# Kernel tuning notes

Hardware: AMD Instinct MI355X
Metric: run time of the kernel (lower is better)

The kernel has to match this reference:

```python
import jax, jax.numpy as jnp
import numpy as np
import math

HIDDEN_DIM = 1024
N_HEAD = 16
HEAD_DIM = HIDDEN_DIM // N_HEAD
BS, SEQ = 2, 4096


def setup_inputs() -> dict:
    key = jax.random.key(0)
    ks = jax.random.split(key, 6)
    s = 1.0 / math.sqrt(HIDDEN_DIM)
    return {
        "x": jax.random.normal(ks[0], (BS, SEQ, HIDDEN_DIM), dtype=jnp.float32),
        "attention_mask": jnp.zeros((1, 1, SEQ, SEQ), dtype=jnp.float32),
        "wq_w": jax.random.normal(ks[1], (HIDDEN_DIM, HIDDEN_DIM), dtype=jnp.float32) * s,
        "wq_b": jnp.zeros((HIDDEN_DIM,), dtype=jnp.float32),
        "wk_w": jax.random.normal(ks[2], (HIDDEN_DIM, HIDDEN_DIM), dtype=jnp.float32) * s,
        "wk_b": jnp.zeros((HIDDEN_DIM,), dtype=jnp.float32),
        "wv_w": jax.random.normal(ks[3], (HIDDEN_DIM, HIDDEN_DIM), dtype=jnp.float32) * s,
        "wv_b": jnp.zeros((HIDDEN_DIM,), dtype=jnp.float32),
        "wo_w": jax.random.normal(ks[4], (HIDDEN_DIM, HIDDEN_DIM), dtype=jnp.float32) * s,
        "wo_b": jnp.zeros((HIDDEN_DIM,), dtype=jnp.float32),
    }


def reference(x, attention_mask, wq_w, wq_b, wk_w, wk_b, wv_w, wv_b, wo_w, wo_b):
    bs, seq_len, _ = x.shape
    # nn.Linear: y = x @ W.T + b
    Q = x @ wq_w.T + wq_b
    K = x @ wk_w.T + wk_b
    V = x @ wv_w.T + wv_b
    # [bs, n_head, seq, head_dim]
    Q = Q.reshape(bs, seq_len, N_HEAD, HEAD_DIM).transpose(0, 2, 1, 3)
    K = K.reshape(bs, seq_len, N_HEAD, HEAD_DIM).transpose(0, 2, 1, 3)
    V = V.reshape(bs, seq_len, N_HEAD, HEAD_DIM).transpose(0, 2, 1, 3)
    scale = 1.0 / math.sqrt(HEAD_DIM)
    att = jnp.einsum('bhqd,bhkd->bhqk', Q, K) * scale
    att = att + attention_mask
    att = jax.nn.softmax(att, axis=-1)
    # dropout is identity in eval mode (p=0.1 during training)
    out = jnp.einsum('bhqk,bhkd->bhqd', att, V)
    out = out.transpose(0, 2, 1, 3).reshape(bs, seq_len, HIDDEN_DIM)
    return out @ wo_w.T + wo_b
```

## Files before the change

### kernel.cpp

```cpp
#include <hip/hip_runtime.h>

typedef unsigned short u16;
typedef __bf16 bf16x4 __attribute__((ext_vector_type(4)));
typedef __bf16 bf16x8 __attribute__((ext_vector_type(8)));
typedef float f32x4 __attribute__((ext_vector_type(4)));

#define SEQ_LEN 4096
#define HID 1024
#define NHEAD 16
#define HDIM 64
#define MROWS 8192
#define LOG2E 1.44269504088896f

__device__ __forceinline__ u16 f2bf(float f) {
  union { float f; unsigned u; } v; v.f = f;
  unsigned r = v.u + 0x7fffu + ((v.u >> 16) & 1u);
  return (u16)(r >> 16);
}

__device__ __forceinline__ float fexp2(float x) {
  float r;
  asm("v_exp_f32 %0, %1" : "=v"(r) : "v"(x));
  return r;
}

__device__ __forceinline__ bf16x8 pack8(f32x4 a, f32x4 b) {
  union { unsigned u[4]; bf16x8 v; } r;
  asm("v_cvt_pk_bf16_f32 %0, %1, %2" : "=v"(r.u[0]) : "v"(a[0]), "v"(a[1]));
  asm("v_cvt_pk_bf16_f32 %0, %1, %2" : "=v"(r.u[1]) : "v"(a[2]), "v"(a[3]));
  asm("v_cvt_pk_bf16_f32 %0, %1, %2" : "=v"(r.u[2]) : "v"(b[0]), "v"(b[1]));
  asm("v_cvt_pk_bf16_f32 %0, %1, %2" : "=v"(r.u[3]) : "v"(b[2]), "v"(b[3]));
  return r.v;
}

__device__ __forceinline__ void gload16(const void* g, void* lds) {
  __builtin_amdgcn_global_load_lds((const __attribute__((address_space(1))) void*)g,
                                   (__attribute__((address_space(3))) void*)lds, 16, 0, 0);
}


__global__ void prep_kernel(const float* __restrict__ x,
                            const float* __restrict__ w0, const float* __restrict__ w1,
                            const float* __restrict__ w2, const float* __restrict__ w3,
                            const float* __restrict__ mask,
                            u16* __restrict__ xb, u16* __restrict__ wb, int* __restrict__ flag) {
  const int NX = MROWS * HID / 4;
  const int NW = HID * HID / 4;
  const int NM = SEQ_LEN * SEQ_LEN / 4;
  const int TOT = NX + 4 * NW + NM;
  int stride = gridDim.x * blockDim.x;
  bool nz = false;
  for (int i = blockIdx.x * blockDim.x + threadIdx.x; i < TOT; i += stride) {
    if (i < NX) {
      float4 v = ((const float4*)x)[i];
      ((ushort4*)xb)[i] = make_ushort4(f2bf(v.x), f2bf(v.y), f2bf(v.z), f2bf(v.w));
    } else if (i < NX + 4 * NW) {
      int j = i - NX;
      int mat = j >> 18;
      int off = j & (NW - 1);
      const float* src = (mat == 0) ? w0 : (mat == 1) ? w1 : (mat == 2) ? w2 : w3;
      float4 v = ((const float4*)src)[off];
      ((ushort4*)(wb + (size_t)mat * HID * HID))[off] =
          make_ushort4(f2bf(v.x), f2bf(v.y), f2bf(v.z), f2bf(v.w));
    } else {
      int j = i - NX - 4 * NW;
      float4 v = ((const float4*)mask)[j];
      nz |= (v.x != 0.f) | (v.y != 0.f) | (v.z != 0.f) | (v.w != 0.f);
    }
  }
  if (__any(nz) && (threadIdx.x & 63) == 0) atomicOr(flag, 1);
}


__device__ __forceinline__ void gemm_core(const u16* __restrict__ A, const u16* __restrict__ W,
                                          int m0, int n0, char* As, char* Bs, f32x4 acc[4][4]) {
  const int t = threadIdx.x, w = t >> 6, l = t & 63;
  const int lr = l & 15, lg = l >> 4;
  const int wr = (w >> 1) * 64, wc = (w & 1) * 64;
#pragma unroll
  for (int i = 0; i < 4; i++)
#pragma unroll
    for (int j = 0; j < 4; j++) acc[i][j] = (f32x4){0.f, 0.f, 0.f, 0.f};

  for (int k0 = 0; k0 < HID; k0 += 64) {
    __syncthreads();
#pragma unroll
    for (int j = 0; j < 4; j++) {
      int o = w * 4096 + j * 1024 + l * 16;
      int row = o >> 7, kb = (o >> 4) & 7, skb = kb ^ (row & 7);
      gload16(A + (size_t)(m0 + row) * HID + k0 + skb * 8, As + (w * 4096 + j * 1024));
      gload16(W + (size_t)(n0 + row) * HID + k0 + skb * 8, Bs + (w * 4096 + j * 1024));
    }
    __syncthreads();
#pragma unroll
    for (int ks = 0; ks < 2; ks++) {
      bf16x8 af[4], bf[4];
      int kb = ks * 4 + lg;
#pragma unroll
      for (int mt = 0; mt < 4; mt++) {
        int row = wr + mt * 16 + lr;
        af[mt] = *(const bf16x8*)(As + row * 128 + ((kb ^ (row & 7)) << 4));
      }
#pragma unroll
      for (int nt = 0; nt < 4; nt++) {
        int row = wc + nt * 16 + lr;
        bf[nt] = *(const bf16x8*)(Bs + row * 128 + ((kb ^ (row & 7)) << 4));
      }
#pragma unroll
      for (int mt = 0; mt < 4; mt++)
#pragma unroll
        for (int nt = 0; nt < 4; nt++)
          acc[mt][nt] = __builtin_amdgcn_mfma_f32_16x16x32_bf16(af[mt], bf[nt], acc[mt][nt], 0, 0, 0);
    }
  }
}

__global__ __launch_bounds__(256) void gemm_qkv_kernel(
    const u16* __restrict__ xb, const u16* __restrict__ wqb, const u16* __restrict__ wkb,
    const u16* __restrict__ wvb, const float* __restrict__ bq, const float* __restrict__ bk,
    const float* __restrict__ bv, u16* __restrict__ Qb, u16* __restrict__ Kb, u16* __restrict__ VT) {
  __shared__ __align__(128) char lds[32768];
  int flat = blockIdx.y * 64 + blockIdx.x;
  int xcd = flat & 7, j = flat >> 3;
  int bx = xcd * 8 + (j & 7);
  int by = j >> 3;
  int m0 = bx * 128;
  int ng = by * 128;
  int mat = ng >> 10, n0 = ng & 1023;
  const u16* W = (mat == 0) ? wqb : (mat == 1) ? wkb : wvb;
  const float* bias = (mat == 0) ? bq : (mat == 1) ? bk : bv;
  f32x4 acc[4][4];
  gemm_core(xb, W, m0, n0, lds, lds + 16384, acc);

  const int t = threadIdx.x, w = t >> 6, l = t & 63;
  const int lr = l & 15, lg = l >> 4;
  if (mat < 2) {
    u16* dst = (mat == 0) ? Qb : Kb;
    float scale = (mat == 0) ? 0.125f * LOG2E : 1.0f;
#pragma unroll
    for (int mt = 0; mt < 4; mt++)
#pragma unroll
      for (int nt = 0; nt < 4; nt++) {
        int n = n0 + (w & 1) * 64 + nt * 16 + lr;
        float bn = bias[n];
#pragma unroll
        for (int i = 0; i < 4; i++) {
          int m = m0 + (w >> 1) * 64 + mt * 16 + lg * 4 + i;
          dst[(size_t)m * HID + n] = f2bf((acc[mt][nt][i] + bn) * scale);
        }
      }
  } else {
#pragma unroll
    for (int mt = 0; mt < 4; mt++)
#pragma unroll
      for (int nt = 0; nt < 4; nt++) {
        int m = m0 + (w >> 1) * 64 + mt * 16 + lg * 4;
        int n = n0 + (w & 1) * 64 + nt * 16 + lr;
        int b = m >> 12, s = m & 4095;
        int h = n >> 6, d = n & 63;
        int t4 = (s >> 2) & 15;
        int t4p = ((t4 & 8)) | ((t4 & 3) << 1) | ((t4 >> 2) & 1);
        int sp = (s & ~63) | (t4p << 2);
        float bn = bias[n];
        ushort4 pk = make_ushort4(f2bf(acc[mt][nt][0] + bn), f2bf(acc[mt][nt][1] + bn),
                                  f2bf(acc[mt][nt][2] + bn), f2bf(acc[mt][nt][3] + bn));
        *(ushort4*)(VT + (((size_t)(b * NHEAD + h) * HDIM + d) * SEQ_LEN + sp)) = pk;
      }
  }
}

__global__ __launch_bounds__(256) void gemm_out_kernel(
    const u16* __restrict__ Ob, const u16* __restrict__ wob, const float* __restrict__ bo,
    float* __restrict__ out) {
  __shared__ __align__(128) char lds[32768];
  int flat = blockIdx.y * 64 + blockIdx.x;
  int xcd = flat & 7, j = flat >> 3;
  int bx = xcd * 8 + (j & 7);
  int by = j >> 3;
  int m0 = bx * 128, n0 = by * 128;
  f32x4 acc[4][4];
  gemm_core(Ob, wob, m0, n0, lds, lds + 16384, acc);
  const int t = threadIdx.x, w = t >> 6, l = t & 63;
  const int lr = l & 15, lg = l >> 4;
#pragma unroll
  for (int mt = 0; mt < 4; mt++)
#pragma unroll
    for (int nt = 0; nt < 4; nt++) {
      int n = n0 + (w & 1) * 64 + nt * 16 + lr;
      float bn = bo[n];
#pragma unroll
      for (int i = 0; i < 4; i++) {
        int m = m0 + (w >> 1) * 64 + mt * 16 + lg * 4 + i;
        out[(size_t)m * HID + n] = acc[mt][nt][i] + bn;
      }
    }
}

__global__ __launch_bounds__(256, 2) void attn_kernel(
    const u16* __restrict__ Qb, const u16* __restrict__ Kb, const u16* __restrict__ VT,
    const float* __restrict__ mask, const int* __restrict__ flag, u16* __restrict__ Ob) {
  __shared__ __align__(128) char lds[32768];
  const int flat = blockIdx.x;
  const int xcd = flat & 7;
  const int slot = flat >> 3;
  const int bh = xcd * 4 + (slot >> 4);
  const int bx = slot & 15;
  const int q0 = bx * 256;
  const int b = bh >> 4, h = bh & 15;
  const int t = threadIdx.x, w = t >> 6, l = t & 63;
  const int lr = l & 15, lg = l >> 4;
  const bool useMask = (flag[0] != 0);
  int qrow[4];
#pragma unroll
  for (int s = 0; s < 4; s++) qrow[s] = q0 + w * 64 + s * 16 + lr;

  bf16x8 qf[4][2];
#pragma unroll
  for (int s = 0; s < 4; s++) {
    const u16* qp = Qb + (size_t)(b * SEQ_LEN + qrow[s]) * HID + h * HDIM;
#pragma unroll
    for (int ks = 0; ks < 2; ks++) qf[s][ks] = *(const bf16x8*)(qp + (ks * 4 + lg) * 8);
  }

  bf16x8 ones;
#pragma unroll
  for (int j = 0; j < 8; j++) ones[j] = (__bf16)1.0f;

  f32x4 oacc[4][4];
#pragma unroll
  for (int s = 0; s < 4; s++)
#pragma unroll
    for (int dt = 0; dt < 4; dt++) oacc[s][dt] = (f32x4){0.f, 0.f, 0.f, 0.f};
  f32x4 lacc[4];
#pragma unroll
  for (int s = 0; s < 4; s++) lacc[s] = (f32x4){0.f, 0.f, 0.f, 0.f};
  float m_r[4] = {-1e30f, -1e30f, -1e30f, -1e30f};

  int off[2][4];
#pragma unroll
  for (int ks = 0; ks < 2; ks++) {
    int kb = ks * 4 + lg;
#pragma unroll
    for (int kt = 0; kt < 4; kt++) {
      int row = kt * 16 + lr;
      off[ks][kt] = row * 128 + ((kb ^ (row & 7)) << 4);
    }
  }

  const int o0 = t * 16;
  const int o1 = o0 + 4096;
  const int r0 = t >> 3;
  const int r1 = r0 + 32;
  const int sk0 = (t & 7) ^ (r0 & 7);
  const int sk1 = (t & 7) ^ (r1 & 7);
  const u16* kg0 = Kb + (size_t)(b * SEQ_LEN) * HID + h * HDIM + (size_t)r0 * HID + sk0 * 8;
  const u16* kg1 = Kb + (size_t)(b * SEQ_LEN) * HID + h * HDIM + (size_t)r1 * HID + sk1 * 8;
  const u16* vg0 = VT + ((size_t)(b * NHEAD + h) * HDIM + r0) * SEQ_LEN + sk0 * 8;
  const u16* vg1 = VT + ((size_t)(b * NHEAD + h) * HDIM + r1) * SEQ_LEN + sk1 * 8;

#define STAGE(BI)                                            \
  do {                                                       \
    gload16(kg0, lds + (BI) * 8192 + o0);                    \
    gload16(kg1, lds + (BI) * 8192 + o1);                    \
    gload16(vg0, lds + 16384 + (BI) * 8192 + o0);            \
    gload16(vg1, lds + 16384 + (BI) * 8192 + o1);            \
    kg0 += 64 * HID; kg1 += 64 * HID; vg0 += 64; vg1 += 64;  \
  } while (0)

#define HALF_HEAD(Ks, H)                                                                   \
    bf16x8 kf[2][2];                                                                       \
    _Pragma("unroll") for (int ks = 0; ks < 2; ks++)                                       \
    _Pragma("unroll") for (int ktl = 0; ktl < 2; ktl++)                                    \
        kf[ks][ktl] = *(const bf16x8*)((Ks) + off[ks][2 * (H) + ktl]);                     \
    f32x4 sf[4][2];                                                                        \
    _Pragma("unroll") for (int s = 0; s < 4; s++)                                          \
    _Pragma("unroll") for (int ktl = 0; ktl < 2; ktl++) sf[s][ktl] = (f32x4){0,0,0,0};     \
    __builtin_amdgcn_s_setprio(1);                                                         \
    _Pragma("unroll") for (int ks = 0; ks < 2; ks++)                                       \
    _Pragma("unroll") for (int s = 0; s < 4; s++)                                          \
    _Pragma("unroll") for (int ktl = 0; ktl < 2; ktl++)                                    \
        sf[s][ktl] = __builtin_amdgcn_mfma_f32_16x16x32_bf16(kf[ks][ktl], qf[s][ks],       \
                                                             sf[s][ktl], 0, 0, 0);        \
    __builtin_amdgcn_s_setprio(0);

#define HALF_TAIL(Vs, H)                                                                   \
    bf16x8 vf[4];                                                                          \
    _Pragma("unroll") for (int dt = 0; dt < 4; dt++)                                       \
        vf[dt] = *(const bf16x8*)((Vs) + off[H][dt]);                                      \
    bf16x8 pb[4];                                                                          \
    _Pragma("unroll") for (int s = 0; s < 4; s++)                                          \
        pb[s] = pack8(sf[s][0], sf[s][1]);                                                 \
    __builtin_amdgcn_s_setprio(1);                                                         \
    _Pragma("unroll") for (int s = 0; s < 4; s++) {                                        \
      _Pragma("unroll") for (int dt = 0; dt < 4; dt++)                                     \
          oacc[s][dt] =                                                                    \
              __builtin_amdgcn_mfma_f32_16x16x32_bf16(vf[dt], pb[s], oacc[s][dt], 0,0,0);  \
      lacc[s] = __builtin_amdgcn_mfma_f32_16x16x32_bf16(ones, pb[s], lacc[s], 0, 0, 0);    \
    }                                                                                      \
    __builtin_amdgcn_s_setprio(0);

#define HALF_FAST(BI, H)                                                                   \
  do {                                                                                     \
    const char* Ks = lds + (BI) * 8192;                                                    \
    const char* Vs = lds + 16384 + (BI) * 8192;                                            \
    HALF_HEAD(Ks, H)                                                                       \
    _Pragma("unroll") for (int s = 0; s < 4; s++)                                          \
    _Pragma("unroll") for (int ktl = 0; ktl < 2; ktl++)                                    \
    _Pragma("unroll") for (int i = 0; i < 4; i++)                                          \
        sf[s][ktl][i] = fexp2(sf[s][ktl][i]);                                              \
    HALF_TAIL(Vs, H)                                                                       \
  } while (0)

#define HALF_SAFE(BI, H, KV0)                                                              \
  do {                                                                                     \
    const char* Ks = lds + (BI) * 8192;                                                    \
    const char* Vs = lds + 16384 + (BI) * 8192;                                            \
    HALF_HEAD(Ks, H)                                                                       \
    _Pragma("unroll") for (int s = 0; s < 4; s++)                                          \
    _Pragma("unroll") for (int ktl = 0; ktl < 2; ktl++)                                    \
    _Pragma("unroll") for (int i = 0; i < 4; i++)                                          \
        sf[s][ktl][i] += mask[(size_t)qrow[s] * SEQ_LEN + (KV0) + (2 * (H) + ktl) * 16 +   \
                              lg * 4 + i] * LOG2E;                                         \
    float mx[4];                                                                           \
    _Pragma("unroll") for (int s = 0; s < 4; s++) {                                        \
      float m1 = fmaxf(fmaxf(sf[s][0][0], sf[s][0][1]), sf[s][0][2]);                      \
      m1 = fmaxf(fmaxf(m1, sf[s][0][3]), sf[s][1][0]);                                     \
      m1 = fmaxf(fmaxf(m1, sf[s][1][1]), sf[s][1][2]);                                     \
      m1 = fmaxf(m1, sf[s][1][3]);                                                         \
      m1 = fmaxf(m1, __shfl_xor(m1, 16));                                                  \
      mx[s] = fmaxf(m1, __shfl_xor(m1, 32));                                               \
    }                                                                                      \
    float dmax = fmaxf(fmaxf(mx[0] - m_r[0], mx[1] - m_r[1]),                              \
                       fmaxf(mx[2] - m_r[2], mx[3] - m_r[3]));                             \
    if (__any(dmax > 8.0f)) {                                                              \
      _Pragma("unroll") for (int s = 0; s < 4; s++) {                                      \
        float nm = fmaxf(m_r[s], mx[s]);                                                   \
        float scf = fexp2(m_r[s] - nm);                                                    \
        m_r[s] = nm;                                                                       \
        _Pragma("unroll") for (int dt = 0; dt < 4; dt++)                                   \
        _Pragma("unroll") for (int i = 0; i < 4; i++) oacc[s][dt][i] *= scf;               \
        lacc[s] *= scf;                                                                    \
      }                                                                                    \
    }                                                                                      \
    _Pragma("unroll") for (int s = 0; s < 4; s++)                                          \
    _Pragma("unroll") for (int ktl = 0; ktl < 2; ktl++)                                    \
    _Pragma("unroll") for (int i = 0; i < 4; i++)                                          \
        sf[s][ktl][i] = fexp2(sf[s][ktl][i] - m_r[s]);                                     \
    HALF_TAIL(Vs, H)                                                                       \
  } while (0)

  STAGE(0);
  __syncthreads();

  const int NT = SEQ_LEN / 64;
  if (!useMask) {
    for (int t2 = 0; t2 < NT / 2; ++t2) {
      STAGE(1);
      HALF_FAST(0, 0);
      HALF_FAST(0, 1);
      __syncthreads();
      if (t2 != NT / 2 - 1) STAGE(0);
      HALF_FAST(1, 0);
      HALF_FAST(1, 1);
      __syncthreads();
    }
  } else {
    for (int t2 = 0; t2 < NT / 2; ++t2) {
      STAGE(1);
      HALF_SAFE(0, 0, t2 * 128);
      HALF_SAFE(0, 1, t2 * 128);
      __syncthreads();
      if (t2 != NT / 2 - 1) STAGE(0);
      HALF_SAFE(1, 0, t2 * 128 + 64);
      HALF_SAFE(1, 1, t2 * 128 + 64);
      __syncthreads();
    }
  }
#undef STAGE
#undef HALF_HEAD
#undef HALF_TAIL
#undef HALF_FAST
#undef HALF_SAFE

#pragma unroll
  for (int s = 0; s < 4; s++) {
    float inv = 1.0f / lacc[s][0];
    u16* orow = Ob + (size_t)(b * SEQ_LEN + qrow[s]) * HID + h * HDIM;
#pragma unroll
    for (int dt = 0; dt < 4; dt++) {
      ushort4 pk = make_ushort4(f2bf(oacc[s][dt][0] * inv), f2bf(oacc[s][dt][1] * inv),
                                f2bf(oacc[s][dt][2] * inv), f2bf(oacc[s][dt][3] * inv));
      *(ushort4*)(orow + dt * 16 + lg * 4) = pk;
    }
  }
}


extern "C" void kernel_launch(void* const* d_in, const int* in_sizes, int n_in,
                              void* d_out, int out_size, void* d_ws, size_t ws_size,
                              hipStream_t stream) {
  const float* x    = (const float*)d_in[0];
  const float* mask = (const float*)d_in[1];
  const float* wq   = (const float*)d_in[2];
  const float* bq   = (const float*)d_in[3];
  const float* wk   = (const float*)d_in[4];
  const float* bk   = (const float*)d_in[5];
  const float* wv   = (const float*)d_in[6];
  const float* bv   = (const float*)d_in[7];
  const float* wo   = (const float*)d_in[8];
  const float* bo   = (const float*)d_in[9];

  char* ws = (char*)d_ws;
  u16* xb  = (u16*)(ws + 0);
  u16* wqb = (u16*)(ws + 16777216);
  u16* Qb  = (u16*)(ws + 25165824);
  u16* Kb  = (u16*)(ws + 41943040);
  u16* VT  = (u16*)(ws + 58720256);
  int* flag = (int*)(ws + 75497472);
  u16* wkb = wqb + 1048576;
  u16* wvb = wqb + 2097152;
  u16* wob = wqb + 3145728;
  u16* Ob = xb;

  (void)hipMemsetAsync(flag, 0, 4, stream);
  prep_kernel<<<2048, 256, 0, stream>>>(x, wq, wk, wv, wo, mask, xb, wqb, flag);
  gemm_qkv_kernel<<<dim3(64, 24), 256, 0, stream>>>(xb, wqb, wkb, wvb, bq, bk, bv, Qb, Kb, VT);
  attn_kernel<<<512, 256, 0, stream>>>(Qb, Kb, VT, mask, flag, Ob);
  gemm_out_kernel<<<dim3(64, 8), 256, 0, stream>>>(Ob, wob, bo, (float*)d_out);
}
```

Measured before the change: 230.9 us.

## Move mask scan into QKV GEMM and double attention KV stage size

The 64MB attention-mask zero check moves out of the prep kernel and into the QKV GEMM prologue, split evenly across all GEMM blocks, so it is spread over a compute-bound kernel instead of lengthening the bandwidth-bound prep pass. The attention kernel now stages 128 KV rows per buffer instead of 64, using 64KB of LDS, which halves the number of barriers and stage issues per KV sweep. The larger LDS footprint may limit the kernel to fewer resident blocks per CU than the launch bounds request, and the mask scan adds memory traffic ahead of each GEMM block.

```diff
diff --git a/kernel.cpp b/kernel.cpp
--- a/kernel.cpp
+++ b/kernel.cpp
@@ -42,19 +42,16 @@
 __global__ void prep_kernel(const float* __restrict__ x,
                             const float* __restrict__ w0, const float* __restrict__ w1,
                             const float* __restrict__ w2, const float* __restrict__ w3,
-                            const float* __restrict__ mask,
-                            u16* __restrict__ xb, u16* __restrict__ wb, int* __restrict__ flag) {
+                            u16* __restrict__ xb, u16* __restrict__ wb) {
   const int NX = MROWS * HID / 4;
   const int NW = HID * HID / 4;
-  const int NM = SEQ_LEN * SEQ_LEN / 4;
-  const int TOT = NX + 4 * NW + NM;
+  const int TOT = NX + 4 * NW;
   int stride = gridDim.x * blockDim.x;
-  bool nz = false;
   for (int i = blockIdx.x * blockDim.x + threadIdx.x; i < TOT; i += stride) {
     if (i < NX) {
       float4 v = ((const float4*)x)[i];
       ((ushort4*)xb)[i] = make_ushort4(f2bf(v.x), f2bf(v.y), f2bf(v.z), f2bf(v.w));
-    } else if (i < NX + 4 * NW) {
+    } else {
       int j = i - NX;
       int mat = j >> 18;
       int off = j & (NW - 1);
@@ -62,13 +59,8 @@
       float4 v = ((const float4*)src)[off];
       ((ushort4*)(wb + (size_t)mat * HID * HID))[off] =
           make_ushort4(f2bf(v.x), f2bf(v.y), f2bf(v.z), f2bf(v.w));
-    } else {
-      int j = i - NX - 4 * NW;
-      float4 v = ((const float4*)mask)[j];
-      nz |= (v.x != 0.f) | (v.y != 0.f) | (v.z != 0.f) | (v.w != 0.f);
-    }
-  }
-  if (__any(nz) && (threadIdx.x & 63) == 0) atomicOr(flag, 1);
+    }
+  }
 }
 
 
@@ -118,7 +110,8 @@
 __global__ __launch_bounds__(256) void gemm_qkv_kernel(
     const u16* __restrict__ xb, const u16* __restrict__ wqb, const u16* __restrict__ wkb,
     const u16* __restrict__ wvb, const float* __restrict__ bq, const float* __restrict__ bk,
-    const float* __restrict__ bv, u16* __restrict__ Qb, u16* __restrict__ Kb, u16* __restrict__ VT) {
+    const float* __restrict__ bv, const float* __restrict__ mask, int* __restrict__ flag,
+    u16* __restrict__ Qb, u16* __restrict__ Kb, u16* __restrict__ VT) {
   __shared__ __align__(128) char lds[32768];
   int flat = blockIdx.y * 64 + blockIdx.x;
   int xcd = flat & 7, j = flat >> 3;
@@ -129,6 +122,21 @@
   int mat = ng >> 10, n0 = ng & 1023;
   const u16* W = (mat == 0) ? wqb : (mat == 1) ? wkb : wvb;
   const float* bias = (mat == 0) ? bq : (mat == 1) ? bk : bv;
+
+  {
+    const int NM = SEQ_LEN * SEQ_LEN / 4;
+    const int nblk = 64 * 24;
+    int per = (NM + nblk - 1) / nblk;
+    int base = flat * per;
+    int end = base + per < NM ? base + per : NM;
+    bool nz = false;
+    for (int i = base + threadIdx.x; i < end; i += 256) {
+      float4 v = ((const float4*)mask)[i];
+      nz |= (v.x != 0.f) | (v.y != 0.f) | (v.z != 0.f) | (v.w != 0.f);
+    }
+    if (__any(nz) && (threadIdx.x & 63) == 0) atomicOr(flag, 1);
+  }
+
   f32x4 acc[4][4];
   gemm_core(xb, W, m0, n0, lds, lds + 16384, acc);
 
@@ -199,7 +207,7 @@
 __global__ __launch_bounds__(256, 2) void attn_kernel(
     const u16* __restrict__ Qb, const u16* __restrict__ Kb, const u16* __restrict__ VT,
     const float* __restrict__ mask, const int* __restrict__ flag, u16* __restrict__ Ob) {
-  __shared__ __align__(128) char lds[32768];
+  __shared__ __align__(128) char lds[65536];
   const int flat = blockIdx.x;
   const int xcd = flat & 7;
   const int slot = flat >> 3;
@@ -258,13 +266,17 @@
   const u16* vg0 = VT + ((size_t)(b * NHEAD + h) * HDIM + r0) * SEQ_LEN + sk0 * 8;
   const u16* vg1 = VT + ((size_t)(b * NHEAD + h) * HDIM + r1) * SEQ_LEN + sk1 * 8;
 
-#define STAGE(BI)                                            \
-  do {                                                       \
-    gload16(kg0, lds + (BI) * 8192 + o0);                    \
-    gload16(kg1, lds + (BI) * 8192 + o1);                    \
-    gload16(vg0, lds + 16384 + (BI) * 8192 + o0);            \
-    gload16(vg1, lds + 16384 + (BI) * 8192 + o1);            \
-    kg0 += 64 * HID; kg1 += 64 * HID; vg0 += 64; vg1 += 64;  \
+#define STAGE(BI)                                                  \
+  do {                                                             \
+    gload16(kg0, lds + (BI) * 32768 + o0);                         \
+    gload16(kg1, lds + (BI) * 32768 + o1);                         \
+    gload16(kg0 + 64 * HID, lds + (BI) * 32768 + 8192 + o0);       \
+    gload16(kg1 + 64 * HID, lds + (BI) * 32768 + 8192 + o1);       \
+    gload16(vg0, lds + (BI) * 32768 + 16384 + o0);                 \
+    gload16(vg1, lds + (BI) * 32768 + 16384 + o1);                 \
+    gload16(vg0 + 64, lds + (BI) * 32768 + 24576 + o0);            \
+    gload16(vg1 + 64, lds + (BI) * 32768 + 24576 + o1);            \
+    kg0 += 128 * HID; kg1 += 128 * HID; vg0 += 128; vg1 += 128;    \
   } while (0)
 
 #define HALF_HEAD(Ks, H)                                                                   \
@@ -299,10 +311,10 @@
     }                                                                                      \
     __builtin_amdgcn_s_setprio(0);
 
-#define HALF_FAST(BI, H)                                                                   \
+#define HALF_FAST(BI, T, H)                                                                \
   do {                                                                                     \
-    const char* Ks = lds + (BI) * 8192;                                                    \
-    const char* Vs = lds + 16384 + (BI) * 8192;                                            \
+    const char* Ks = lds + (BI) * 32768 + (T) * 8192;                                      \
+    const char* Vs = lds + (BI) * 32768 + 16384 + (T) * 8192;                              \
     HALF_HEAD(Ks, H)                                                                       \
     _Pragma("unroll") for (int s = 0; s < 4; s++)                                          \
     _Pragma("unroll") for (int ktl = 0; ktl < 2; ktl++)                                    \
@@ -311,16 +323,16 @@
     HALF_TAIL(Vs, H)                                                                       \
   } while (0)
 
-#define HALF_SAFE(BI, H, KV0)                                                              \
+#define HALF_SAFE(BI, T, H, KV0)                                                           \
   do {                                                                                     \
-    const char* Ks = lds + (BI) * 8192;                                                    \
-    const char* Vs = lds + 16384 + (BI) * 8192;                                            \
+    const char* Ks = lds + (BI) * 32768 + (T) * 8192;                                      \
+    const char* Vs = lds + (BI) * 32768 + 16384 + (T) * 8192;                              \
     HALF_HEAD(Ks, H)                                                                       \
     _Pragma("unroll") for (int s = 0; s < 4; s++)                                          \
     _Pragma("unroll") for (int ktl = 0; ktl < 2; ktl++)                                    \
     _Pragma("unroll") for (int i = 0; i < 4; i++)                                          \
-        sf[s][ktl][i] += mask[(size_t)qrow[s] * SEQ_LEN + (KV0) + (2 * (H) + ktl) * 16 +   \
-                              lg * 4 + i] * LOG2E;                                         \
+        sf[s][ktl][i] += mask[(size_t)qrow[s] * SEQ_LEN + (KV0) + (T) * 64 +               \
+                              (2 * (H) + ktl) * 16 + lg * 4 + i] * LOG2E;                  \
     float mx[4];                                                                           \
     _Pragma("unroll") for (int s = 0; s < 4; s++) {                                        \
       float m1 = fmaxf(fmaxf(sf[s][0][0], sf[s][0][1]), sf[s][0][2]);                      \
@@ -352,27 +364,28 @@
   STAGE(0);
   __syncthreads();
 
-  const int NT = SEQ_LEN / 64;
+  const int NT2 = SEQ_LEN / 128;
   if (!useMask) {
-    for (int t2 = 0; t2 < NT / 2; ++t2) {
+    for (int t2 = 0; t2 < NT2 / 2; ++t2) {
       STAGE(1);
-      HALF_FAST(0, 0);
-      HALF_FAST(0, 1);
+      HALF_FAST(0, 0, 0); HALF_FAST(0, 0, 1);
+      HALF_FAST(0, 1, 0); HALF_FAST(0, 1, 1);
       __syncthreads();
-      if (t2 != NT / 2 - 1) STAGE(0);
-      HALF_FAST(1, 0);
-      HALF_FAST(1, 1);
+      if (t2 != NT2 / 2 - 1) STAGE(0);
+      HALF_FAST(1, 0, 0); HALF_FAST(1, 0, 1);
+      HALF_FAST(1, 1, 0); HALF_FAST(1, 1, 1);
       __syncthreads();
     }
   } else {
-    for (int t2 = 0; t2 < NT / 2; ++t2) {
+    for (int t2 = 0; t2 < NT2 / 2; ++t2) {
+      int kv0 = t2 * 256;
       STAGE(1);
-      HALF_SAFE(0, 0, t2 * 128);
-      HALF_SAFE(0, 1, t2 * 128);
+      HALF_SAFE(0, 0, 0, kv0); HALF_SAFE(0, 0, 1, kv0);
+      HALF_SAFE(0, 1, 0, kv0); HALF_SAFE(0, 1, 1, kv0);
       __syncthreads();
-      if (t2 != NT / 2 - 1) STAGE(0);
-      HALF_SAFE(1, 0, t2 * 128 + 64);
-      HALF_SAFE(1, 1, t2 * 128 + 64);
+      if (t2 != NT2 / 2 - 1) STAGE(0);
+      HALF_SAFE(1, 0, 0, kv0 + 128); HALF_SAFE(1, 0, 1, kv0 + 128);
+      HALF_SAFE(1, 1, 0, kv0 + 128); HALF_SAFE(1, 1, 1, kv0 + 128);
       __syncthreads();
     }
   }
@@ -423,8 +436,9 @@
   u16* Ob = xb;
 
   (void)hipMemsetAsync(flag, 0, 4, stream);
-  prep_kernel<<<2048, 256, 0, stream>>>(x, wq, wk, wv, wo, mask, xb, wqb, flag);
-  gemm_qkv_kernel<<<dim3(64, 24), 256, 0, stream>>>(xb, wqb, wkb, wvb, bq, bk, bv, Qb, Kb, VT);
+  prep_kernel<<<2048, 256, 0, stream>>>(x, wq, wk, wv, wo, xb, wqb);
+  gemm_qkv_kernel<<<dim3(64, 24), 256, 0, stream>>>(xb, wqb, wkb, wvb, bq, bk, bv, mask, flag,
+                                                    Qb, Kb, VT);
   attn_kernel<<<512, 256, 0, stream>>>(Qb, Kb, VT, mask, flag, Ob);
   gemm_out_kernel<<<dim3(64, 8), 256, 0, stream>>>(Ob, wob, bo, (float*)d_out);
 }
```

Measured after the change: 234.5 us. Within noise of the previous version (+1.5%).
